# Optimization experiments

Measured on AMD Instinct MI355X. Metric: run time of the kernel, lower is better.

Reference implementation:

```python
import jax, jax.numpy as jnp
import numpy as np

N_EMBD = 2048
N_HEAD = 16
N_KV_HEAD = 4
HEAD_DIM = N_EMBD // N_HEAD  # 128
N_REP = N_HEAD // N_KV_HEAD  # 4
ROPE_BASE = 1000000.0
B, T = 2, 2048


def _rotate_half(x):
    x1, x2 = jnp.split(x, 2, axis=-1)
    return jnp.concatenate([-x2, x1], axis=-1)


def _rope(q, k, t):
    # q: [b,t,h,d], k: [b,t,kvh,d]; full rotary (partial_rotary_factor=1.0)
    pos = jnp.arange(t, dtype=jnp.float32)
    inv_freq = 1.0 / (ROPE_BASE ** (jnp.arange(0, HEAD_DIM, 2, dtype=jnp.float32) / HEAD_DIM))
    ang = pos[:, None] * inv_freq[None, :]                      # [t, d/2]
    cos = jnp.concatenate([jnp.cos(ang), jnp.cos(ang)], -1)     # [t, d]
    sin = jnp.concatenate([jnp.sin(ang), jnp.sin(ang)], -1)
    cos = cos[None, :, None, :]
    sin = sin[None, :, None, :]
    q = q * cos + _rotate_half(q) * sin
    k = k * cos + _rotate_half(k) * sin
    return q, k


def setup_inputs() -> dict:
    key = jax.random.key(0)
    ks = jax.random.split(key, 9)
    std = 0.02
    proj_std = 0.02 / np.sqrt(2 * 24)
    return {
        "x": jax.random.normal(ks[0], (B, T, N_EMBD), dtype=jnp.float32),
        "Wq": jax.random.normal(ks[1], (N_EMBD, N_HEAD * HEAD_DIM), dtype=jnp.float32) * std,
        "bq": jnp.zeros((N_HEAD * HEAD_DIM,), dtype=jnp.float32),
        "Wk": jax.random.normal(ks[2], (N_EMBD, N_KV_HEAD * HEAD_DIM), dtype=jnp.float32) * std,
        "bk": jnp.zeros((N_KV_HEAD * HEAD_DIM,), dtype=jnp.float32),
        "Wv": jax.random.normal(ks[3], (N_EMBD, N_KV_HEAD * HEAD_DIM), dtype=jnp.float32) * std,
        "bv": jnp.zeros((N_KV_HEAD * HEAD_DIM,), dtype=jnp.float32),
        "Wo": jax.random.normal(ks[4], (N_EMBD, N_EMBD), dtype=jnp.float32) * proj_std,
        "bo": jnp.zeros((N_EMBD,), dtype=jnp.float32),
    }


def reference(x, Wq, bq, Wk, bk, Wv, bv, Wo, bo):
    b, t, _ = x.shape
    q = (x @ Wq + bq).reshape(b, t, N_HEAD, HEAD_DIM)
    k = (x @ Wk + bk).reshape(b, t, N_KV_HEAD, HEAD_DIM)
    v = (x @ Wv + bv).reshape(b, t, N_KV_HEAD, HEAD_DIM)
    q, k = _rope(q, k, t)
    # repeat_kv: expand kv heads by n_rep
    k = jnp.broadcast_to(k[:, :, :, None, :], (b, t, N_KV_HEAD, N_REP, HEAD_DIM)).reshape(b, t, N_HEAD, HEAD_DIM)
    v = jnp.broadcast_to(v[:, :, :, None, :], (b, t, N_KV_HEAD, N_REP, HEAD_DIM)).reshape(b, t, N_HEAD, HEAD_DIM)
    qh = q.transpose(0, 2, 1, 3)  # [b,h,t,d]
    kh = k.transpose(0, 2, 1, 3)
    vh = v.transpose(0, 2, 1, 3)
    causal = jnp.tril(jnp.ones((t, t), dtype=bool))[None, None]  # [1,1,t,t]
    bias = jnp.where(causal, 0.0, -1e9).astype(jnp.float32)
    scores = jnp.einsum('bhtd,bhTd->bhtT', qh, kh) / jnp.sqrt(jnp.float32(HEAD_DIM))
    attn_w = jax.nn.softmax(scores + bias, axis=-1)
    attn_out = jnp.einsum('bhtT,bhTd->bhtd', attn_w, vh)
    attn = attn_out.transpose(0, 2, 1, 3).reshape(b, t, N_EMBD)
    return attn @ Wo + bo
```

## Files before the change

kernel.cpp:

```cpp
#include <hip/hip_runtime.h>

typedef _Float16 f16x8 __attribute__((ext_vector_type(8)));
typedef _Float16 f16x4 __attribute__((ext_vector_type(4)));
typedef float    f32x4 __attribute__((ext_vector_type(4)));

__device__ __forceinline__ void gload16(const void* g, void* l) {
  __builtin_amdgcn_global_load_lds((const __attribute__((address_space(1))) void*)g,
                                   (__attribute__((address_space(3))) void*)l, 16, 0, 0);
}

__global__ __launch_bounds__(256) void cast_f32_f16(const float* __restrict__ src,
                                                    _Float16* __restrict__ dst, int n4) {
  int i = blockIdx.x * 256 + threadIdx.x;
  if (i < n4) {
    f32x4 v = *(const f32x4*)(src + (size_t)i * 4);
    f16x4 o;
    o[0] = (_Float16)v[0]; o[1] = (_Float16)v[1];
    o[2] = (_Float16)v[2]; o[3] = (_Float16)v[3];
    *(f16x4*)(dst + (size_t)i * 4) = o;
  }
}

__global__ __launch_bounds__(256) void wqkvtrans_kernel(const float* __restrict__ Wq,
                                                        const float* __restrict__ Wk,
                                                        const float* __restrict__ Wv,
                                                        _Float16* __restrict__ dst) {
  const int n0 = blockIdx.x * 64, k0 = blockIdx.y * 64;
  const float* src; int N, nb;
  if (n0 < 2048)      { src = Wq; N = 2048; nb = n0; }
  else if (n0 < 2560) { src = Wk; N = 512;  nb = n0 - 2048; }
  else                { src = Wv; N = 512;  nb = n0 - 2560; }
  __shared__ float tile[64][65];
#pragma unroll
  for (int i = 0; i < 16; ++i) {
    int id = i * 256 + threadIdx.x;
    int kk = id >> 6, nn = id & 63;
    tile[kk][nn] = src[(size_t)(k0 + kk) * N + nb + nn];
  }
  __syncthreads();
#pragma unroll
  for (int i = 0; i < 16; ++i) {
    int id = i * 256 + threadIdx.x;
    int nn = id >> 6, kk = id & 63;
    dst[(size_t)(n0 + nn) * 2048 + k0 + kk] = (_Float16)tile[kk][nn];
  }
}

__global__ __launch_bounds__(256) void wtrans_kernel(const float* __restrict__ src,
                                                     _Float16* __restrict__ dst,
                                                     int N, int K, int rowOff, int ldDst) {
  const int n0 = blockIdx.x * 64, k0 = blockIdx.y * 64;
  __shared__ float tile[64][65];
#pragma unroll
  for (int i = 0; i < 16; ++i) {
    int id = i * 256 + threadIdx.x;
    int kk = id >> 6, nn = id & 63;
    tile[kk][nn] = src[(size_t)(k0 + kk) * N + n0 + nn];
  }
  __syncthreads();
#pragma unroll
  for (int i = 0; i < 16; ++i) {
    int id = i * 256 + threadIdx.x;
    int nn = id >> 6, kk = id & 63;
    dst[(size_t)(rowOff + n0 + nn) * ldDst + k0 + kk] = (_Float16)tile[kk][nn];
  }
}

__global__ __launch_bounds__(256) void biaspack_kernel(const float* __restrict__ bq,
                                                       const float* __restrict__ bk,
                                                       const float* __restrict__ bv,
                                                       float* __restrict__ out) {
  int i = blockIdx.x * 256 + threadIdx.x;
  if (i < 3072) out[i] = (i < 2048) ? bq[i] : (i < 2560 ? bk[i - 2048] : bv[i - 2560]);
}

template <bool F16OUT>
__global__ __launch_bounds__(256) void gemm_nt(const _Float16* __restrict__ A,
                                               const _Float16* __restrict__ B,
                                               const float* __restrict__ bias,
                                               void* __restrict__ Cv,
                                               int M, int N, int K) {
  __shared__ __align__(16) _Float16 As[128][64];
  __shared__ __align__(16) _Float16 Bs[128][64];
  const int tid = threadIdx.x;
  const int lane = tid & 63, wave = tid >> 6;
  const int wr = wave >> 1, wc = wave & 1;
  const int r = lane & 15, g = lane >> 4;
  const int rb = blockIdx.y * 128, cb = blockIdx.x * 128;

  const int swz = ((tid & 7) ^ ((tid >> 3) & 7)) * 8;
  const _Float16* aSrc = A + (size_t)(rb + (tid >> 3)) * K + swz;
  const _Float16* bSrc = B + (size_t)(cb + (tid >> 3)) * K + swz;

  f32x4 acc[4][4] = {};

  for (int kt = 0; kt < K; kt += 64) {
    __syncthreads();
#pragma unroll
    for (int p = 0; p < 4; ++p) {
      gload16(aSrc + (size_t)(p * 32) * K + kt, (_Float16*)As + (p * 256 + wave * 64) * 8);
      gload16(bSrc + (size_t)(p * 32) * K + kt, (_Float16*)Bs + (p * 256 + wave * 64) * 8);
    }
    __syncthreads();
#pragma unroll
    for (int kk = 0; kk < 2; ++kk) {
      f16x8 af[4], bf[4];
#pragma unroll
      for (int m = 0; m < 4; ++m) {
        int row = wr * 64 + m * 16 + r;
        af[m] = *(const f16x8*)(&As[row][((kk * 4 + g) ^ (row & 7)) * 8]);
      }
#pragma unroll
      for (int n = 0; n < 4; ++n) {
        int row = wc * 64 + n * 16 + r;
        bf[n] = *(const f16x8*)(&Bs[row][((kk * 4 + g) ^ (row & 7)) * 8]);
      }
#pragma unroll
      for (int m = 0; m < 4; ++m)
#pragma unroll
        for (int n = 0; n < 4; ++n)
          acc[m][n] = __builtin_amdgcn_mfma_f32_16x16x32_f16(af[m], bf[n], acc[m][n], 0, 0, 0);
    }
  }

  float bvals[4];
#pragma unroll
  for (int n = 0; n < 4; ++n) bvals[n] = bias[cb + wc * 64 + n * 16 + r];
#pragma unroll
  for (int m = 0; m < 4; ++m) {
#pragma unroll
    for (int n = 0; n < 4; ++n) {
#pragma unroll
      for (int j = 0; j < 4; ++j) {
        int row = rb + wr * 64 + m * 16 + g * 4 + j;
        int col = cb + wc * 64 + n * 16 + r;
        float v = acc[m][n][j] + bvals[n];
        if (F16OUT)
          ((_Float16*)Cv)[(size_t)row * N + col] = (_Float16)v;
        else
          ((float*)Cv)[(size_t)row * N + col] = v;
      }
    }
  }
}

__global__ __launch_bounds__(256) void rope_kernel(_Float16* __restrict__ QKV) {
  const int tok = blockIdx.x;
  const int t = tok & 2047;
  __shared__ float cs[64], sn[64];
  if (threadIdx.x < 64) {
    int j = threadIdx.x;
    float freq = exp2f((float)(-2 * j) * (19.931568569324174f / 128.0f));
    float ang = (float)t * freq;
    cs[j] = cosf(ang);
    sn[j] = sinf(ang);
  }
  __syncthreads();
  _Float16* base = QKV + (size_t)tok * 3072;
  int idx = threadIdx.x;
  if (idx < 160) {
    int head = idx >> 3, j0 = (idx & 7) * 8;
    int cb = (head < 16) ? head * 128 : 2048 + (head - 16) * 128;
    _Float16* p = base + cb;
    f16x8 a = *(const f16x8*)(p + j0);
    f16x8 b2 = *(const f16x8*)(p + 64 + j0);
    f16x8 oa, ob;
#pragma unroll
    for (int e = 0; e < 8; ++e) {
      float c = cs[j0 + e], s = sn[j0 + e];
      float x1 = (float)a[e], x2 = (float)b2[e];
      oa[e] = (_Float16)(x1 * c - x2 * s);
      ob[e] = (_Float16)(x2 * c + x1 * s);
    }
    *(f16x8*)(p + j0) = oa;
    *(f16x8*)(p + 64 + j0) = ob;
  }
}

__global__ __launch_bounds__(256) void vtrans_kernel(const _Float16* __restrict__ QKV,
                                                     _Float16* __restrict__ Vt) {
  const int bk = blockIdx.z;
  const int t0 = blockIdx.x * 64, d0 = blockIdx.y * 64;
  const int b = bk >> 2, kvh = bk & 3;
  __shared__ _Float16 tile[64][65];
  const _Float16* src = QKV + (size_t)b * 2048 * 3072 + 2560 + kvh * 128;
#pragma unroll
  for (int i = 0; i < 16; ++i) {
    int id = i * 256 + threadIdx.x;
    int tt = id >> 6, dd = id & 63;
    tile[tt][dd] = src[(size_t)(t0 + tt) * 3072 + d0 + dd];
  }
  __syncthreads();
  _Float16* dst = Vt + (size_t)bk * 128 * 2048;
#pragma unroll
  for (int i = 0; i < 16; ++i) {
    int id = i * 256 + threadIdx.x;
    int dd = id >> 6, tt = id & 63;
    dst[(size_t)(d0 + dd) * 2048 + t0 + tt] = tile[tt][dd];
  }
}

__global__ __launch_bounds__(512) void attn_kernel(const _Float16* __restrict__ QKV,
                                                   const _Float16* __restrict__ Vt,
                                                   _Float16* __restrict__ O) {
  const int bid = blockIdx.x;
  const int b = bid >> 8;
  const int ii = bid & 255;
  const int h = ii >> 4;
  const int qtr = ii & 15;
  const int qt = b ? 15 - qtr : qtr;
  const int tid = threadIdx.x;
  const int wave = tid >> 6, lane = tid & 63;
  const int r = lane & 15, g = lane >> 4;
  const int q0 = qt * 128 + wave * 16;
  const int kvh = h >> 2;
  const _Float16* Qb  = QKV + (size_t)b * 2048 * 3072 + h * 128;
  const _Float16* Kb  = QKV + (size_t)b * 2048 * 3072 + 2048 + kvh * 128;
  const _Float16* Vtg = Vt + (size_t)(b * 4 + kvh) * 128 * 2048;

  __shared__ __align__(16) _Float16 Klds[2][64][128];
  __shared__ __align__(16) _Float16 Vlds[2][128][64];
  __shared__ __align__(16) _Float16 Plds[8][16][64];

  const _Float16* kSrc = Kb  + (size_t)(tid >> 4) * 3072 + (((tid & 15) ^ ((tid >> 4) & 7)) * 8);
  const _Float16* vSrc = Vtg + (size_t)(tid >> 3) * 2048 + (((tid & 7) ^ ((tid >> 3) & 7)) * 8);

  f16x8 qf[4];
  {
    const float qsc = 0.08838834764831845f * 1.4426950408889634f;
    const _Float16* qrow = Qb + (size_t)(q0 + r) * 3072 + g * 8;
#pragma unroll
    for (int c = 0; c < 4; ++c) {
      f16x8 v = *(const f16x8*)(qrow + c * 32);
#pragma unroll
      for (int i = 0; i < 8; ++i) v[i] = (_Float16)((float)v[i] * qsc);
      qf[c] = v;
    }
  }
  asm volatile("s_waitcnt vmcnt(0)" ::: "memory");

  f32x4 oacc[8] = {};
  float mrun = -1e30f, lrun = 0.f;
  const int kend = qt * 128 + 128;
  const int qlim = q0 + 16;

  {
    gload16(kSrc,                          &Klds[0][0][0] + (wave * 64) * 8);
    gload16(kSrc + (size_t)32 * 3072,      &Klds[0][0][0] + (512 + wave * 64) * 8);
    gload16(vSrc,                          &Vlds[0][0][0] + (wave * 64) * 8);
    gload16(vSrc + (size_t)64 * 2048,      &Vlds[0][0][0] + (512 + wave * 64) * 8);
  }

  int cur = 0;
  for (int kb = 0; kb < kend; kb += 64) {
    if (kb + 64 < kend) {
      int nb = kb + 64, nxt = cur ^ 1;
      gload16(kSrc + (size_t)nb * 3072,        &Klds[nxt][0][0] + (wave * 64) * 8);
      gload16(kSrc + (size_t)(nb + 32) * 3072, &Klds[nxt][0][0] + (512 + wave * 64) * 8);
      gload16(vSrc + nb,                       &Vlds[nxt][0][0] + (wave * 64) * 8);
      gload16(vSrc + (size_t)64 * 2048 + nb,   &Vlds[nxt][0][0] + (512 + wave * 64) * 8);
      asm volatile("s_waitcnt vmcnt(4)" ::: "memory");
    } else {
      asm volatile("s_waitcnt vmcnt(0)" ::: "memory");
    }
    __builtin_amdgcn_s_barrier();
    __builtin_amdgcn_sched_barrier(0);
    if (kb < qlim) {
      f32x4 sT[4] = {};
      __builtin_amdgcn_s_setprio(1);
#pragma unroll
      for (int c = 0; c < 4; ++c) {
#pragma unroll
        for (int n = 0; n < 4; ++n) {
          f16x8 kf = *(const f16x8*)(&Klds[cur][n * 16 + r][(((c * 4 + g) ^ (r & 7)) * 8)]);
          sT[n] = __builtin_amdgcn_mfma_f32_16x16x32_f16(kf, qf[c], sT[n], 0, 0, 0);
        }
      }
      __builtin_amdgcn_s_setprio(0);
      if (kb + 63 > q0) {
#pragma unroll
        for (int n = 0; n < 4; ++n)
#pragma unroll
          for (int j = 0; j < 4; ++j) {
            int kg = kb + n * 16 + g * 4 + j;
            if (kg > q0 + r) sT[n][j] = -1e30f;
          }
      }
      float mt = -1e30f;
#pragma unroll
      for (int n = 0; n < 4; ++n)
#pragma unroll
        for (int j = 0; j < 4; ++j) mt = fmaxf(mt, sT[n][j]);
      mt = fmaxf(mt, __shfl_xor(mt, 16));
      mt = fmaxf(mt, __shfl_xor(mt, 32));
      if (__any(mt > mrun)) {
        float mnew = fmaxf(mrun, mt);
        float alpha = exp2f(mrun - mnew);
        lrun *= alpha;
        float al[4];
#pragma unroll
        for (int jj = 0; jj < 4; ++jj) al[jj] = __shfl(alpha, g * 4 + jj);
#pragma unroll
        for (int dt = 0; dt < 8; ++dt)
#pragma unroll
          for (int jj = 0; jj < 4; ++jj) oacc[dt][jj] *= al[jj];
        mrun = mnew;
      }
      float p[4][4];
      float rs = 0.f;
#pragma unroll
      for (int n = 0; n < 4; ++n)
#pragma unroll
        for (int j = 0; j < 4; ++j) {
          p[n][j] = exp2f(sT[n][j] - mrun);
          rs += p[n][j];
        }
      rs += __shfl_xor(rs, 16);
      rs += __shfl_xor(rs, 32);
      lrun += rs;
      asm volatile("" ::: "memory");
#pragma unroll
      for (int n = 0; n < 4; ++n) {
        f16x4 p4;
#pragma unroll
        for (int j = 0; j < 4; ++j) p4[j] = (_Float16)p[n][j];
        int c16s = (2 * n + (g >> 1)) ^ (r & 7);
        *(f16x4*)(&Plds[wave][r][c16s * 8 + (g & 1) * 4]) = p4;
      }
      asm volatile("s_waitcnt lgkmcnt(0)" ::: "memory");
      __builtin_amdgcn_sched_barrier(0);
      f16x8 pa0 = *(const f16x8*)(&Plds[wave][r][((g) ^ (r & 7)) * 8]);
      f16x8 pa1 = *(const f16x8*)(&Plds[wave][r][((4 + g) ^ (r & 7)) * 8]);
      __builtin_amdgcn_s_setprio(1);
#pragma unroll
      for (int dt = 0; dt < 8; ++dt) {
        f16x8 vf0 = *(const f16x8*)(&Vlds[cur][dt * 16 + r][((g) ^ (r & 7)) * 8]);
        oacc[dt] = __builtin_amdgcn_mfma_f32_16x16x32_f16(pa0, vf0, oacc[dt], 0, 0, 0);
        f16x8 vf1 = *(const f16x8*)(&Vlds[cur][dt * 16 + r][((4 + g) ^ (r & 7)) * 8]);
        oacc[dt] = __builtin_amdgcn_mfma_f32_16x16x32_f16(pa1, vf1, oacc[dt], 0, 0, 0);
      }
      __builtin_amdgcn_s_setprio(0);
    }
    __builtin_amdgcn_sched_barrier(0);
    __builtin_amdgcn_s_barrier();
    __builtin_amdgcn_sched_barrier(0);
    cur ^= 1;
  }

  float linv = 1.0f / lrun;
  float li[4];
#pragma unroll
  for (int jj = 0; jj < 4; ++jj) li[jj] = __shfl(linv, g * 4 + jj);
#pragma unroll
  for (int dt = 0; dt < 8; ++dt)
#pragma unroll
    for (int jj = 0; jj < 4; ++jj)
      O[(size_t)(b * 2048 + q0 + g * 4 + jj) * 2048 + h * 128 + dt * 16 + r] =
          (_Float16)(oacc[dt][jj] * li[jj]);
}

extern "C" void kernel_launch(void* const* d_in, const int* in_sizes, int n_in,
                              void* d_out, int out_size, void* d_ws, size_t ws_size,
                              hipStream_t stream) {
  const float* x  = (const float*)d_in[0];
  const float* Wq = (const float*)d_in[1];
  const float* bq = (const float*)d_in[2];
  const float* Wk = (const float*)d_in[3];
  const float* bk = (const float*)d_in[4];
  const float* Wv = (const float*)d_in[5];
  const float* bv = (const float*)d_in[6];
  const float* Wo = (const float*)d_in[7];
  const float* bo = (const float*)d_in[8];
  float* out = (float*)d_out;

  char* ws = (char*)d_ws;
  constexpr size_t QKV_OFF  = 0;
  constexpr size_t VT_OFF   = 25165824;
  constexpr size_t ATTN_OFF = VT_OFF + 4194304;
  constexpr size_t WT_OFF   = ATTN_OFF + 16777216;
  constexpr size_t BIAS_OFF = WT_OFF + 12582912;
  _Float16* QKV  = (_Float16*)(ws + QKV_OFF);
  _Float16* Vt   = (_Float16*)(ws + VT_OFF);
  _Float16* attn = (_Float16*)(ws + ATTN_OFF);
  _Float16* WT   = (_Float16*)(ws + WT_OFF);
  float*    bqkv = (float*)(ws + BIAS_OFF);
  _Float16* xb = (_Float16*)d_out;

  cast_f32_f16<<<8192, 256, 0, stream>>>(x, xb, (2 * 2048 * 2048) / 4);
  wqkvtrans_kernel<<<dim3(48, 32), 256, 0, stream>>>(Wq, Wk, Wv, WT);
  biaspack_kernel<<<12, 256, 0, stream>>>(bq, bk, bv, bqkv);
  gemm_nt<true><<<dim3(3072 / 128, 4096 / 128), 256, 0, stream>>>(xb, WT, bqkv, QKV, 4096, 3072, 2048);
  wtrans_kernel<<<dim3(32, 32), 256, 0, stream>>>(Wo, WT, 2048, 2048, 0, 2048);
  rope_kernel<<<4096, 256, 0, stream>>>(QKV);
  vtrans_kernel<<<dim3(32, 2, 8), 256, 0, stream>>>(QKV, Vt);
  attn_kernel<<<512, 512, 0, stream>>>(QKV, Vt, attn);
  gemm_nt<false><<<dim3(2048 / 128, 4096 / 128), 256, 0, stream>>>(attn, WT, bo, out, 4096, 2048, 2048);
}
```

Before: 216.6 us.

## Switch attention to 32x32x16 MFMA with 4 waves of 32 query rows

```diff
diff --git a/kernel.cpp b/kernel.cpp
--- a/kernel.cpp
+++ b/kernel.cpp
@@ -3,6 +3,7 @@
 typedef _Float16 f16x8 __attribute__((ext_vector_type(8)));
 typedef _Float16 f16x4 __attribute__((ext_vector_type(4)));
 typedef float    f32x4 __attribute__((ext_vector_type(4)));
+typedef float    f32x16 __attribute__((ext_vector_type(16)));
 
 __device__ __forceinline__ void gload16(const void* g, void* l) {
   __builtin_amdgcn_global_load_lds((const __attribute__((address_space(1))) void*)g,
@@ -200,7 +201,7 @@
   }
 }
 
-__global__ __launch_bounds__(512) void attn_kernel(const _Float16* __restrict__ QKV,
+__global__ __launch_bounds__(256) void attn_kernel(const _Float16* __restrict__ QKV,
                                                    const _Float16* __restrict__ Vt,
                                                    _Float16* __restrict__ O) {
   const int bid = blockIdx.x;
@@ -211,152 +212,133 @@
   const int qt = b ? 15 - qtr : qtr;
   const int tid = threadIdx.x;
   const int wave = tid >> 6, lane = tid & 63;
-  const int r = lane & 15, g = lane >> 4;
-  const int q0 = qt * 128 + wave * 16;
+  const int l31 = lane & 31, hi = lane >> 5;
+  const int q0w = qt * 128 + wave * 32;
   const int kvh = h >> 2;
   const _Float16* Qb  = QKV + (size_t)b * 2048 * 3072 + h * 128;
   const _Float16* Kb  = QKV + (size_t)b * 2048 * 3072 + 2048 + kvh * 128;
   const _Float16* Vtg = Vt + (size_t)(b * 4 + kvh) * 128 * 2048;
 
-  __shared__ __align__(16) _Float16 Klds[2][64][128];
-  __shared__ __align__(16) _Float16 Vlds[2][128][64];
-  __shared__ __align__(16) _Float16 Plds[8][16][64];
+  __shared__ __align__(16) _Float16 Klds[64][128];
+  __shared__ __align__(16) _Float16 Vlds[128][64];
+  __shared__ __align__(16) _Float16 Plds[4][32][64];
 
   const _Float16* kSrc = Kb  + (size_t)(tid >> 4) * 3072 + (((tid & 15) ^ ((tid >> 4) & 7)) * 8);
   const _Float16* vSrc = Vtg + (size_t)(tid >> 3) * 2048 + (((tid & 7) ^ ((tid >> 3) & 7)) * 8);
 
-  f16x8 qf[4];
+  f16x8 qf[8];
   {
     const float qsc = 0.08838834764831845f * 1.4426950408889634f;
-    const _Float16* qrow = Qb + (size_t)(q0 + r) * 3072 + g * 8;
-#pragma unroll
-    for (int c = 0; c < 4; ++c) {
-      f16x8 v = *(const f16x8*)(qrow + c * 32);
-#pragma unroll
-      for (int i = 0; i < 8; ++i) v[i] = (_Float16)((float)v[i] * qsc);
-      qf[c] = v;
-    }
-  }
-  asm volatile("s_waitcnt vmcnt(0)" ::: "memory");
-
-  f32x4 oacc[8] = {};
+    const _Float16* qrow = Qb + (size_t)(q0w + l31) * 3072 + hi * 8;
+#pragma unroll
+    for (int ds = 0; ds < 8; ++ds) {
+      f16x8 v = *(const f16x8*)(qrow + ds * 16);
+#pragma unroll
+      for (int e = 0; e < 8; ++e) v[e] = (_Float16)((float)v[e] * qsc);
+      qf[ds] = v;
+    }
+  }
+
+  f32x16 oacc[4] = {};
   float mrun = -1e30f, lrun = 0.f;
   const int kend = qt * 128 + 128;
-  const int qlim = q0 + 16;
-
-  {
-    gload16(kSrc,                          &Klds[0][0][0] + (wave * 64) * 8);
-    gload16(kSrc + (size_t)32 * 3072,      &Klds[0][0][0] + (512 + wave * 64) * 8);
-    gload16(vSrc,                          &Vlds[0][0][0] + (wave * 64) * 8);
-    gload16(vSrc + (size_t)64 * 2048,      &Vlds[0][0][0] + (512 + wave * 64) * 8);
-  }
-
-  int cur = 0;
+  const int qlim = q0w + 32;
+
   for (int kb = 0; kb < kend; kb += 64) {
-    if (kb + 64 < kend) {
-      int nb = kb + 64, nxt = cur ^ 1;
-      gload16(kSrc + (size_t)nb * 3072,        &Klds[nxt][0][0] + (wave * 64) * 8);
-      gload16(kSrc + (size_t)(nb + 32) * 3072, &Klds[nxt][0][0] + (512 + wave * 64) * 8);
-      gload16(vSrc + nb,                       &Vlds[nxt][0][0] + (wave * 64) * 8);
-      gload16(vSrc + (size_t)64 * 2048 + nb,   &Vlds[nxt][0][0] + (512 + wave * 64) * 8);
-      asm volatile("s_waitcnt vmcnt(4)" ::: "memory");
-    } else {
-      asm volatile("s_waitcnt vmcnt(0)" ::: "memory");
-    }
-    __builtin_amdgcn_s_barrier();
-    __builtin_amdgcn_sched_barrier(0);
+#pragma unroll
+    for (int p = 0; p < 4; ++p) {
+      gload16(kSrc + (size_t)(kb + p * 16) * 3072, (_Float16*)Klds + (p * 256 + tid) * 8);
+      gload16(vSrc + (size_t)(p * 32) * 2048 + kb, (_Float16*)Vlds + (p * 256 + tid) * 8);
+    }
+    __syncthreads();
     if (kb < qlim) {
-      f32x4 sT[4] = {};
+      f32x16 sT[2] = {};
       __builtin_amdgcn_s_setprio(1);
 #pragma unroll
-      for (int c = 0; c < 4; ++c) {
-#pragma unroll
-        for (int n = 0; n < 4; ++n) {
-          f16x8 kf = *(const f16x8*)(&Klds[cur][n * 16 + r][(((c * 4 + g) ^ (r & 7)) * 8)]);
-          sT[n] = __builtin_amdgcn_mfma_f32_16x16x32_f16(kf, qf[c], sT[n], 0, 0, 0);
+      for (int ds = 0; ds < 8; ++ds) {
+#pragma unroll
+        for (int ks = 0; ks < 2; ++ks) {
+          f16x8 kf = *(const f16x8*)(&Klds[ks * 32 + l31][(((ds * 2 + hi) ^ (l31 & 7)) * 8)]);
+          sT[ks] = __builtin_amdgcn_mfma_f32_32x32x16_f16(kf, qf[ds], sT[ks], 0, 0, 0);
         }
       }
       __builtin_amdgcn_s_setprio(0);
-      if (kb + 63 > q0) {
-#pragma unroll
-        for (int n = 0; n < 4; ++n)
-#pragma unroll
-          for (int j = 0; j < 4; ++j) {
-            int kg = kb + n * 16 + g * 4 + j;
-            if (kg > q0 + r) sT[n][j] = -1e30f;
+      if (kb + 63 > q0w) {
+#pragma unroll
+        for (int ks = 0; ks < 2; ++ks)
+#pragma unroll
+          for (int r = 0; r < 16; ++r) {
+            int kg = kb + ks * 32 + (r & 3) + 8 * (r >> 2) + 4 * hi;
+            if (kg > q0w + l31) sT[ks][r] = -1e30f;
           }
       }
       float mt = -1e30f;
 #pragma unroll
-      for (int n = 0; n < 4; ++n)
-#pragma unroll
-        for (int j = 0; j < 4; ++j) mt = fmaxf(mt, sT[n][j]);
-      mt = fmaxf(mt, __shfl_xor(mt, 16));
+      for (int ks = 0; ks < 2; ++ks)
+#pragma unroll
+        for (int r = 0; r < 16; ++r) mt = fmaxf(mt, sT[ks][r]);
       mt = fmaxf(mt, __shfl_xor(mt, 32));
       if (__any(mt > mrun)) {
         float mnew = fmaxf(mrun, mt);
         float alpha = exp2f(mrun - mnew);
         lrun *= alpha;
-        float al[4];
-#pragma unroll
-        for (int jj = 0; jj < 4; ++jj) al[jj] = __shfl(alpha, g * 4 + jj);
-#pragma unroll
-        for (int dt = 0; dt < 8; ++dt)
-#pragma unroll
-          for (int jj = 0; jj < 4; ++jj) oacc[dt][jj] *= al[jj];
+#pragma unroll
+        for (int r = 0; r < 16; ++r) {
+          float al = __shfl(alpha, (r & 3) + 8 * (r >> 2) + 4 * hi);
+#pragma unroll
+          for (int dsub = 0; dsub < 4; ++dsub) oacc[dsub][r] *= al;
+        }
         mrun = mnew;
       }
-      float p[4][4];
+      float pv[2][16];
       float rs = 0.f;
 #pragma unroll
-      for (int n = 0; n < 4; ++n)
-#pragma unroll
-        for (int j = 0; j < 4; ++j) {
-          p[n][j] = exp2f(sT[n][j] - mrun);
-          rs += p[n][j];
-        }
-      rs += __shfl_xor(rs, 16);
+      for (int ks = 0; ks < 2; ++ks)
+#pragma unroll
+        for (int r = 0; r < 16; ++r) {
+          pv[ks][r] = exp2f(sT[ks][r] - mrun);
+          rs += pv[ks][r];
+        }
       rs += __shfl_xor(rs, 32);
       lrun += rs;
       asm volatile("" ::: "memory");
 #pragma unroll
-      for (int n = 0; n < 4; ++n) {
-        f16x4 p4;
-#pragma unroll
-        for (int j = 0; j < 4; ++j) p4[j] = (_Float16)p[n][j];
-        int c16s = (2 * n + (g >> 1)) ^ (r & 7);
-        *(f16x4*)(&Plds[wave][r][c16s * 8 + (g & 1) * 4]) = p4;
-      }
+      for (int ks = 0; ks < 2; ++ks)
+#pragma unroll
+        for (int m = 0; m < 4; ++m) {
+          f16x4 w;
+#pragma unroll
+          for (int j = 0; j < 4; ++j) w[j] = (_Float16)pv[ks][m * 4 + j];
+          int c = (ks * 4 + m) ^ (l31 & 7);
+          *(f16x4*)(&Plds[wave][l31][c * 8 + hi * 4]) = w;
+        }
       asm volatile("s_waitcnt lgkmcnt(0)" ::: "memory");
       __builtin_amdgcn_sched_barrier(0);
-      f16x8 pa0 = *(const f16x8*)(&Plds[wave][r][((g) ^ (r & 7)) * 8]);
-      f16x8 pa1 = *(const f16x8*)(&Plds[wave][r][((4 + g) ^ (r & 7)) * 8]);
       __builtin_amdgcn_s_setprio(1);
 #pragma unroll
-      for (int dt = 0; dt < 8; ++dt) {
-        f16x8 vf0 = *(const f16x8*)(&Vlds[cur][dt * 16 + r][((g) ^ (r & 7)) * 8]);
-        oacc[dt] = __builtin_amdgcn_mfma_f32_16x16x32_f16(pa0, vf0, oacc[dt], 0, 0, 0);
-        f16x8 vf1 = *(const f16x8*)(&Vlds[cur][dt * 16 + r][((4 + g) ^ (r & 7)) * 8]);
-        oacc[dt] = __builtin_amdgcn_mfma_f32_16x16x32_f16(pa1, vf1, oacc[dt], 0, 0, 0);
+      for (int s = 0; s < 4; ++s) {
+        f16x8 pa = *(const f16x8*)(&Plds[wave][l31][(((s * 2 + hi) ^ (l31 & 7)) * 8)]);
+#pragma unroll
+        for (int dsub = 0; dsub < 4; ++dsub) {
+          f16x8 vf = *(const f16x8*)(&Vlds[dsub * 32 + l31][(((s * 2 + hi) ^ (l31 & 7)) * 8)]);
+          oacc[dsub] = __builtin_amdgcn_mfma_f32_32x32x16_f16(pa, vf, oacc[dsub], 0, 0, 0);
+        }
       }
       __builtin_amdgcn_s_setprio(0);
     }
-    __builtin_amdgcn_sched_barrier(0);
-    __builtin_amdgcn_s_barrier();
-    __builtin_amdgcn_sched_barrier(0);
-    cur ^= 1;
+    __syncthreads();
   }
 
   float linv = 1.0f / lrun;
-  float li[4];
-#pragma unroll
-  for (int jj = 0; jj < 4; ++jj) li[jj] = __shfl(linv, g * 4 + jj);
-#pragma unroll
-  for (int dt = 0; dt < 8; ++dt)
-#pragma unroll
-    for (int jj = 0; jj < 4; ++jj)
-      O[(size_t)(b * 2048 + q0 + g * 4 + jj) * 2048 + h * 128 + dt * 16 + r] =
-          (_Float16)(oacc[dt][jj] * li[jj]);
+#pragma unroll
+  for (int r = 0; r < 16; ++r) {
+    int qrow = (r & 3) + 8 * (r >> 2) + 4 * hi;
+    float li = __shfl(linv, qrow);
+    _Float16* orow = O + (size_t)(b * 2048 + q0w + qrow) * 2048 + h * 128 + l31;
+#pragma unroll
+    for (int dsub = 0; dsub < 4; ++dsub)
+      orow[dsub * 32] = (_Float16)(oacc[dsub][r] * li);
+  }
 }
 
 extern "C" void kernel_launch(void* const* d_in, const int* in_sizes, int n_in,
@@ -393,6 +375,6 @@
   wtrans_kernel<<<dim3(32, 32), 256, 0, stream>>>(Wo, WT, 2048, 2048, 0, 2048);
   rope_kernel<<<4096, 256, 0, stream>>>(QKV);
   vtrans_kernel<<<dim3(32, 2, 8), 256, 0, stream>>>(QKV, Vt);
-  attn_kernel<<<512, 512, 0, stream>>>(QKV, Vt, attn);
+  attn_kernel<<<512, 256, 0, stream>>>(QKV, Vt, attn);
   gemm_nt<false><<<dim3(2048 / 128, 4096 / 128), 256, 0, stream>>>(attn, WT, bo, out, 4096, 2048, 2048);
 }
```

After: 277.0 us. 27.9% more time.

## Use persistent atomic work queue with smaller 64-row query tiles in attention

Applied to the files above, without the earlier changes.

```diff
diff --git a/kernel.cpp b/kernel.cpp
--- a/kernel.cpp
+++ b/kernel.cpp
@@ -73,6 +73,8 @@
   int i = blockIdx.x * 256 + threadIdx.x;
   if (i < 3072) out[i] = (i < 2048) ? bq[i] : (i < 2560 ? bk[i - 2048] : bv[i - 2560]);
 }
+
+__global__ void zeroctr_kernel(int* c) { *c = 0; }
 
 template <bool F16OUT>
 __global__ __launch_bounds__(256) void gemm_nt(const _Float16* __restrict__ A,
@@ -200,163 +202,154 @@
   }
 }
 
-__global__ __launch_bounds__(512) void attn_kernel(const _Float16* __restrict__ QKV,
+__global__ __launch_bounds__(256) void attn_kernel(const _Float16* __restrict__ QKV,
                                                    const _Float16* __restrict__ Vt,
-                                                   _Float16* __restrict__ O) {
-  const int bid = blockIdx.x;
-  const int b = bid >> 8;
-  const int ii = bid & 255;
-  const int h = ii >> 4;
-  const int qtr = ii & 15;
-  const int qt = b ? 15 - qtr : qtr;
+                                                   _Float16* __restrict__ O,
+                                                   int* __restrict__ ctr) {
   const int tid = threadIdx.x;
   const int wave = tid >> 6, lane = tid & 63;
   const int r = lane & 15, g = lane >> 4;
-  const int q0 = qt * 128 + wave * 16;
-  const int kvh = h >> 2;
-  const _Float16* Qb  = QKV + (size_t)b * 2048 * 3072 + h * 128;
-  const _Float16* Kb  = QKV + (size_t)b * 2048 * 3072 + 2048 + kvh * 128;
-  const _Float16* Vtg = Vt + (size_t)(b * 4 + kvh) * 128 * 2048;
-
-  __shared__ __align__(16) _Float16 Klds[2][64][128];
-  __shared__ __align__(16) _Float16 Vlds[2][128][64];
-  __shared__ __align__(16) _Float16 Plds[8][16][64];
-
-  const _Float16* kSrc = Kb  + (size_t)(tid >> 4) * 3072 + (((tid & 15) ^ ((tid >> 4) & 7)) * 8);
-  const _Float16* vSrc = Vtg + (size_t)(tid >> 3) * 2048 + (((tid & 7) ^ ((tid >> 3) & 7)) * 8);
-
-  f16x8 qf[4];
-  {
-    const float qsc = 0.08838834764831845f * 1.4426950408889634f;
-    const _Float16* qrow = Qb + (size_t)(q0 + r) * 3072 + g * 8;
-#pragma unroll
-    for (int c = 0; c < 4; ++c) {
-      f16x8 v = *(const f16x8*)(qrow + c * 32);
-#pragma unroll
-      for (int i = 0; i < 8; ++i) v[i] = (_Float16)((float)v[i] * qsc);
-      qf[c] = v;
-    }
-  }
-  asm volatile("s_waitcnt vmcnt(0)" ::: "memory");
-
-  f32x4 oacc[8] = {};
-  float mrun = -1e30f, lrun = 0.f;
-  const int kend = qt * 128 + 128;
-  const int qlim = q0 + 16;
-
-  {
-    gload16(kSrc,                          &Klds[0][0][0] + (wave * 64) * 8);
-    gload16(kSrc + (size_t)32 * 3072,      &Klds[0][0][0] + (512 + wave * 64) * 8);
-    gload16(vSrc,                          &Vlds[0][0][0] + (wave * 64) * 8);
-    gload16(vSrc + (size_t)64 * 2048,      &Vlds[0][0][0] + (512 + wave * 64) * 8);
-  }
-
-  int cur = 0;
-  for (int kb = 0; kb < kend; kb += 64) {
-    if (kb + 64 < kend) {
-      int nb = kb + 64, nxt = cur ^ 1;
-      gload16(kSrc + (size_t)nb * 3072,        &Klds[nxt][0][0] + (wave * 64) * 8);
-      gload16(kSrc + (size_t)(nb + 32) * 3072, &Klds[nxt][0][0] + (512 + wave * 64) * 8);
-      gload16(vSrc + nb,                       &Vlds[nxt][0][0] + (wave * 64) * 8);
-      gload16(vSrc + (size_t)64 * 2048 + nb,   &Vlds[nxt][0][0] + (512 + wave * 64) * 8);
-      asm volatile("s_waitcnt vmcnt(4)" ::: "memory");
-    } else {
-      asm volatile("s_waitcnt vmcnt(0)" ::: "memory");
-    }
-    __builtin_amdgcn_s_barrier();
-    __builtin_amdgcn_sched_barrier(0);
-    if (kb < qlim) {
-      f32x4 sT[4] = {};
-      __builtin_amdgcn_s_setprio(1);
+
+  __shared__ __align__(16) _Float16 Klds[64][128];
+  __shared__ __align__(16) _Float16 Vlds[128][64];
+  __shared__ __align__(16) _Float16 Plds[4][16][64];
+  __shared__ int wslot;
+
+  const int kRowOff = tid >> 4, kChunk = ((tid & 15) ^ ((tid >> 4) & 7)) * 8;
+  const int vRowOff = tid >> 3, vChunk = ((tid & 7) ^ ((tid >> 3) & 7)) * 8;
+
+  for (;;) {
+    __syncthreads();
+    if (tid == 0) wslot = atomicAdd(ctr, 1);
+    __syncthreads();
+    const int w = wslot;
+    if (w >= 1024) break;
+    const int qt = 31 - (w >> 5);
+    const int rem = w & 31;
+    const int b = rem >> 4, h = rem & 15;
+    const int kvh = h >> 2;
+    const int q0 = qt * 64 + wave * 16;
+    const _Float16* Qb  = QKV + (size_t)b * 2048 * 3072 + h * 128;
+    const _Float16* Kb  = QKV + (size_t)b * 2048 * 3072 + 2048 + kvh * 128;
+    const _Float16* Vtg = Vt + (size_t)(b * 4 + kvh) * 128 * 2048;
+    const _Float16* kSrc = Kb  + (size_t)kRowOff * 3072 + kChunk;
+    const _Float16* vSrc = Vtg + (size_t)vRowOff * 2048 + vChunk;
+
+    f16x8 qf[4];
+    {
+      const float qsc = 0.08838834764831845f * 1.4426950408889634f;
+      const _Float16* qrow = Qb + (size_t)(q0 + r) * 3072 + g * 8;
 #pragma unroll
       for (int c = 0; c < 4; ++c) {
+        f16x8 v = *(const f16x8*)(qrow + c * 32);
+#pragma unroll
+        for (int i = 0; i < 8; ++i) v[i] = (_Float16)((float)v[i] * qsc);
+        qf[c] = v;
+      }
+    }
+
+    f32x4 oacc[8] = {};
+    float mrun = -1e30f, lrun = 0.f;
+    const int kend = qt * 64 + 64;
+    const int qlim = q0 + 16;
+
+    for (int kb = 0; kb < kend; kb += 64) {
+#pragma unroll
+      for (int p = 0; p < 4; ++p) {
+        gload16(kSrc + (size_t)(kb + p * 16) * 3072, (_Float16*)Klds + (p * 256 + wave * 64) * 8);
+        gload16(vSrc + (size_t)(p * 32) * 2048 + kb, (_Float16*)Vlds + (p * 256 + wave * 64) * 8);
+      }
+      __syncthreads();
+      if (kb < qlim) {
+        f32x4 sT[4] = {};
+        __builtin_amdgcn_s_setprio(1);
+#pragma unroll
+        for (int c = 0; c < 4; ++c) {
+#pragma unroll
+          for (int n = 0; n < 4; ++n) {
+            f16x8 kf = *(const f16x8*)(&Klds[n * 16 + r][(((c * 4 + g) ^ (r & 7)) * 8)]);
+            sT[n] = __builtin_amdgcn_mfma_f32_16x16x32_f16(kf, qf[c], sT[n], 0, 0, 0);
+          }
+        }
+        __builtin_amdgcn_s_setprio(0);
+        if (kb + 63 > q0) {
+#pragma unroll
+          for (int n = 0; n < 4; ++n)
+#pragma unroll
+            for (int j = 0; j < 4; ++j) {
+              int kg = kb + n * 16 + g * 4 + j;
+              if (kg > q0 + r) sT[n][j] = -1e30f;
+            }
+        }
+        float mt = -1e30f;
+#pragma unroll
+        for (int n = 0; n < 4; ++n)
+#pragma unroll
+          for (int j = 0; j < 4; ++j) mt = fmaxf(mt, sT[n][j]);
+        mt = fmaxf(mt, __shfl_xor(mt, 16));
+        mt = fmaxf(mt, __shfl_xor(mt, 32));
+        if (__any(mt > mrun)) {
+          float mnew = fmaxf(mrun, mt);
+          float alpha = exp2f(mrun - mnew);
+          lrun *= alpha;
+          float al[4];
+#pragma unroll
+          for (int jj = 0; jj < 4; ++jj) al[jj] = __shfl(alpha, g * 4 + jj);
+#pragma unroll
+          for (int dt = 0; dt < 8; ++dt)
+#pragma unroll
+            for (int jj = 0; jj < 4; ++jj) oacc[dt][jj] *= al[jj];
+          mrun = mnew;
+        }
+        float p[4][4];
+        float rs = 0.f;
+#pragma unroll
+        for (int n = 0; n < 4; ++n)
+#pragma unroll
+          for (int j = 0; j < 4; ++j) {
+            p[n][j] = exp2f(sT[n][j] - mrun);
+            rs += p[n][j];
+          }
+        rs += __shfl_xor(rs, 16);
+        rs += __shfl_xor(rs, 32);
+        lrun += rs;
+        asm volatile("" ::: "memory");
 #pragma unroll
         for (int n = 0; n < 4; ++n) {
-          f16x8 kf = *(const f16x8*)(&Klds[cur][n * 16 + r][(((c * 4 + g) ^ (r & 7)) * 8)]);
-          sT[n] = __builtin_amdgcn_mfma_f32_16x16x32_f16(kf, qf[c], sT[n], 0, 0, 0);
-        }
-      }
-      __builtin_amdgcn_s_setprio(0);
-      if (kb + 63 > q0) {
-#pragma unroll
-        for (int n = 0; n < 4; ++n)
-#pragma unroll
-          for (int j = 0; j < 4; ++j) {
-            int kg = kb + n * 16 + g * 4 + j;
-            if (kg > q0 + r) sT[n][j] = -1e30f;
-          }
-      }
-      float mt = -1e30f;
-#pragma unroll
-      for (int n = 0; n < 4; ++n)
-#pragma unroll
-        for (int j = 0; j < 4; ++j) mt = fmaxf(mt, sT[n][j]);
-      mt = fmaxf(mt, __shfl_xor(mt, 16));
-      mt = fmaxf(mt, __shfl_xor(mt, 32));
-      if (__any(mt > mrun)) {
-        float mnew = fmaxf(mrun, mt);
-        float alpha = exp2f(mrun - mnew);
-        lrun *= alpha;
-        float al[4];
-#pragma unroll
-        for (int jj = 0; jj < 4; ++jj) al[jj] = __shfl(alpha, g * 4 + jj);
-#pragma unroll
-        for (int dt = 0; dt < 8; ++dt)
-#pragma unroll
-          for (int jj = 0; jj < 4; ++jj) oacc[dt][jj] *= al[jj];
-        mrun = mnew;
-      }
-      float p[4][4];
-      float rs = 0.f;
-#pragma unroll
-      for (int n = 0; n < 4; ++n)
-#pragma unroll
-        for (int j = 0; j < 4; ++j) {
-          p[n][j] = exp2f(sT[n][j] - mrun);
-          rs += p[n][j];
-        }
-      rs += __shfl_xor(rs, 16);
-      rs += __shfl_xor(rs, 32);
-      lrun += rs;
-      asm volatile("" ::: "memory");
-#pragma unroll
-      for (int n = 0; n < 4; ++n) {
-        f16x4 p4;
-#pragma unroll
-        for (int j = 0; j < 4; ++j) p4[j] = (_Float16)p[n][j];
-        int c16s = (2 * n + (g >> 1)) ^ (r & 7);
-        *(f16x4*)(&Plds[wave][r][c16s * 8 + (g & 1) * 4]) = p4;
-      }
-      asm volatile("s_waitcnt lgkmcnt(0)" ::: "memory");
-      __builtin_amdgcn_sched_barrier(0);
-      f16x8 pa0 = *(const f16x8*)(&Plds[wave][r][((g) ^ (r & 7)) * 8]);
-      f16x8 pa1 = *(const f16x8*)(&Plds[wave][r][((4 + g) ^ (r & 7)) * 8]);
-      __builtin_amdgcn_s_setprio(1);
-#pragma unroll
-      for (int dt = 0; dt < 8; ++dt) {
-        f16x8 vf0 = *(const f16x8*)(&Vlds[cur][dt * 16 + r][((g) ^ (r & 7)) * 8]);
-        oacc[dt] = __builtin_amdgcn_mfma_f32_16x16x32_f16(pa0, vf0, oacc[dt], 0, 0, 0);
-        f16x8 vf1 = *(const f16x8*)(&Vlds[cur][dt * 16 + r][((4 + g) ^ (r & 7)) * 8]);
-        oacc[dt] = __builtin_amdgcn_mfma_f32_16x16x32_f16(pa1, vf1, oacc[dt], 0, 0, 0);
-      }
-      __builtin_amdgcn_s_setprio(0);
-    }
-    __builtin_amdgcn_sched_barrier(0);
-    __builtin_amdgcn_s_barrier();
-    __builtin_amdgcn_sched_barrier(0);
-    cur ^= 1;
-  }
-
-  float linv = 1.0f / lrun;
-  float li[4];
-#pragma unroll
-  for (int jj = 0; jj < 4; ++jj) li[jj] = __shfl(linv, g * 4 + jj);
-#pragma unroll
-  for (int dt = 0; dt < 8; ++dt)
-#pragma unroll
-    for (int jj = 0; jj < 4; ++jj)
-      O[(size_t)(b * 2048 + q0 + g * 4 + jj) * 2048 + h * 128 + dt * 16 + r] =
-          (_Float16)(oacc[dt][jj] * li[jj]);
+          f16x4 p4;
+#pragma unroll
+          for (int j = 0; j < 4; ++j) p4[j] = (_Float16)p[n][j];
+          int c16s = (2 * n + (g >> 1)) ^ (r & 7);
+          *(f16x4*)(&Plds[wave][r][c16s * 8 + (g & 1) * 4]) = p4;
+        }
+        asm volatile("s_waitcnt lgkmcnt(0)" ::: "memory");
+        __builtin_amdgcn_sched_barrier(0);
+        f16x8 pa0 = *(const f16x8*)(&Plds[wave][r][((g) ^ (r & 7)) * 8]);
+        f16x8 pa1 = *(const f16x8*)(&Plds[wave][r][((4 + g) ^ (r & 7)) * 8]);
+        __builtin_amdgcn_s_setprio(1);
+#pragma unroll
+        for (int dt = 0; dt < 8; ++dt) {
+          f16x8 vf0 = *(const f16x8*)(&Vlds[dt * 16 + r][((g) ^ (r & 7)) * 8]);
+          oacc[dt] = __builtin_amdgcn_mfma_f32_16x16x32_f16(pa0, vf0, oacc[dt], 0, 0, 0);
+          f16x8 vf1 = *(const f16x8*)(&Vlds[dt * 16 + r][((4 + g) ^ (r & 7)) * 8]);
+          oacc[dt] = __builtin_amdgcn_mfma_f32_16x16x32_f16(pa1, vf1, oacc[dt], 0, 0, 0);
+        }
+        __builtin_amdgcn_s_setprio(0);
+      }
+      __syncthreads();
+    }
+
+    float linv = 1.0f / lrun;
+    float li[4];
+#pragma unroll
+    for (int jj = 0; jj < 4; ++jj) li[jj] = __shfl(linv, g * 4 + jj);
+#pragma unroll
+    for (int dt = 0; dt < 8; ++dt)
+#pragma unroll
+      for (int jj = 0; jj < 4; ++jj)
+        O[(size_t)(b * 2048 + q0 + g * 4 + jj) * 2048 + h * 128 + dt * 16 + r] =
+            (_Float16)(oacc[dt][jj] * li[jj]);
+  }
 }
 
 extern "C" void kernel_launch(void* const* d_in, const int* in_sizes, int n_in,
@@ -379,20 +372,23 @@
   constexpr size_t ATTN_OFF = VT_OFF + 4194304;
   constexpr size_t WT_OFF   = ATTN_OFF + 16777216;
   constexpr size_t BIAS_OFF = WT_OFF + 12582912;
+  constexpr size_t CTR_OFF  = BIAS_OFF + 12288;
   _Float16* QKV  = (_Float16*)(ws + QKV_OFF);
   _Float16* Vt   = (_Float16*)(ws + VT_OFF);
   _Float16* attn = (_Float16*)(ws + ATTN_OFF);
   _Float16* WT   = (_Float16*)(ws + WT_OFF);
   float*    bqkv = (float*)(ws + BIAS_OFF);
+  int*      ctr  = (int*)(ws + CTR_OFF);
   _Float16* xb = (_Float16*)d_out;
 
   cast_f32_f16<<<8192, 256, 0, stream>>>(x, xb, (2 * 2048 * 2048) / 4);
   wqkvtrans_kernel<<<dim3(48, 32), 256, 0, stream>>>(Wq, Wk, Wv, WT);
   biaspack_kernel<<<12, 256, 0, stream>>>(bq, bk, bv, bqkv);
+  zeroctr_kernel<<<1, 1, 0, stream>>>(ctr);
   gemm_nt<true><<<dim3(3072 / 128, 4096 / 128), 256, 0, stream>>>(xb, WT, bqkv, QKV, 4096, 3072, 2048);
   wtrans_kernel<<<dim3(32, 32), 256, 0, stream>>>(Wo, WT, 2048, 2048, 0, 2048);
   rope_kernel<<<4096, 256, 0, stream>>>(QKV);
   vtrans_kernel<<<dim3(32, 2, 8), 256, 0, stream>>>(QKV, Vt);
-  attn_kernel<<<512, 512, 0, stream>>>(QKV, Vt, attn);
+  attn_kernel<<<1024, 256, 0, stream>>>(QKV, Vt, attn, ctr);
   gemm_nt<false><<<dim3(2048 / 128, 4096 / 128), 256, 0, stream>>>(attn, WT, bo, out, 4096, 2048, 2048);
 }
```

Result: slower. 226.4 us (+4.5%).

## Replace double-buffered 64-key attention tiles with single-buffered 128-key tiles

Applied to the files above, without the earlier changes.

```diff
diff --git a/kernel.cpp b/kernel.cpp
--- a/kernel.cpp
+++ b/kernel.cpp
@@ -218,12 +218,14 @@
   const _Float16* Kb  = QKV + (size_t)b * 2048 * 3072 + 2048 + kvh * 128;
   const _Float16* Vtg = Vt + (size_t)(b * 4 + kvh) * 128 * 2048;
 
-  __shared__ __align__(16) _Float16 Klds[2][64][128];
-  __shared__ __align__(16) _Float16 Vlds[2][128][64];
+  __shared__ __align__(16) _Float16 Klds[128][128];
+  __shared__ __align__(16) _Float16 Vlds[128][128];
   __shared__ __align__(16) _Float16 Plds[8][16][64];
 
-  const _Float16* kSrc = Kb  + (size_t)(tid >> 4) * 3072 + (((tid & 15) ^ ((tid >> 4) & 7)) * 8);
-  const _Float16* vSrc = Vtg + (size_t)(tid >> 3) * 2048 + (((tid & 7) ^ ((tid >> 3) & 7)) * 8);
+  const int sRow = tid >> 4;
+  const int sChunk = ((tid & 15) ^ ((tid >> 4) & 7)) * 8;
+  const _Float16* kSrc = Kb  + (size_t)sRow * 3072 + sChunk;
+  const _Float16* vSrc = Vtg + (size_t)sRow * 2048 + sChunk;
 
   f16x8 qf[4];
   {
@@ -237,52 +239,40 @@
       qf[c] = v;
     }
   }
-  asm volatile("s_waitcnt vmcnt(0)" ::: "memory");
 
   f32x4 oacc[8] = {};
   float mrun = -1e30f, lrun = 0.f;
   const int kend = qt * 128 + 128;
   const int qlim = q0 + 16;
 
-  {
-    gload16(kSrc,                          &Klds[0][0][0] + (wave * 64) * 8);
-    gload16(kSrc + (size_t)32 * 3072,      &Klds[0][0][0] + (512 + wave * 64) * 8);
-    gload16(vSrc,                          &Vlds[0][0][0] + (wave * 64) * 8);
-    gload16(vSrc + (size_t)64 * 2048,      &Vlds[0][0][0] + (512 + wave * 64) * 8);
-  }
-
-  int cur = 0;
-  for (int kb = 0; kb < kend; kb += 64) {
-    if (kb + 64 < kend) {
-      int nb = kb + 64, nxt = cur ^ 1;
-      gload16(kSrc + (size_t)nb * 3072,        &Klds[nxt][0][0] + (wave * 64) * 8);
-      gload16(kSrc + (size_t)(nb + 32) * 3072, &Klds[nxt][0][0] + (512 + wave * 64) * 8);
-      gload16(vSrc + nb,                       &Vlds[nxt][0][0] + (wave * 64) * 8);
-      gload16(vSrc + (size_t)64 * 2048 + nb,   &Vlds[nxt][0][0] + (512 + wave * 64) * 8);
-      asm volatile("s_waitcnt vmcnt(4)" ::: "memory");
-    } else {
-      asm volatile("s_waitcnt vmcnt(0)" ::: "memory");
-    }
-    __builtin_amdgcn_s_barrier();
-    __builtin_amdgcn_sched_barrier(0);
-    if (kb < qlim) {
+  for (int kb = 0; kb < kend; kb += 128) {
+#pragma unroll
+    for (int p = 0; p < 4; ++p) {
+      gload16(kSrc + (size_t)(kb + p * 32) * 3072, (_Float16*)Klds + (p * 512 + tid) * 8);
+      gload16(vSrc + (size_t)(p * 32) * 2048 + kb, (_Float16*)Vlds + (p * 512 + tid) * 8);
+    }
+    __syncthreads();
+#pragma unroll
+    for (int kk2 = 0; kk2 < 128; kk2 += 64) {
+      const int kbb = kb + kk2;
+      if (kbb >= qlim) break;
       f32x4 sT[4] = {};
       __builtin_amdgcn_s_setprio(1);
 #pragma unroll
       for (int c = 0; c < 4; ++c) {
 #pragma unroll
         for (int n = 0; n < 4; ++n) {
-          f16x8 kf = *(const f16x8*)(&Klds[cur][n * 16 + r][(((c * 4 + g) ^ (r & 7)) * 8)]);
+          f16x8 kf = *(const f16x8*)(&Klds[kk2 + n * 16 + r][(((c * 4 + g) ^ (r & 7)) * 8)]);
           sT[n] = __builtin_amdgcn_mfma_f32_16x16x32_f16(kf, qf[c], sT[n], 0, 0, 0);
         }
       }
       __builtin_amdgcn_s_setprio(0);
-      if (kb + 63 > q0) {
+      if (kbb + 63 > q0) {
 #pragma unroll
         for (int n = 0; n < 4; ++n)
 #pragma unroll
           for (int j = 0; j < 4; ++j) {
-            int kg = kb + n * 16 + g * 4 + j;
+            int kg = kbb + n * 16 + g * 4 + j;
             if (kg > q0 + r) sT[n][j] = -1e30f;
           }
       }
@@ -334,17 +324,14 @@
       __builtin_amdgcn_s_setprio(1);
 #pragma unroll
       for (int dt = 0; dt < 8; ++dt) {
-        f16x8 vf0 = *(const f16x8*)(&Vlds[cur][dt * 16 + r][((g) ^ (r & 7)) * 8]);
+        f16x8 vf0 = *(const f16x8*)(&Vlds[dt * 16 + r][((((kk2 >> 3) + g) ^ (r & 7)) * 8)]);
         oacc[dt] = __builtin_amdgcn_mfma_f32_16x16x32_f16(pa0, vf0, oacc[dt], 0, 0, 0);
-        f16x8 vf1 = *(const f16x8*)(&Vlds[cur][dt * 16 + r][((4 + g) ^ (r & 7)) * 8]);
+        f16x8 vf1 = *(const f16x8*)(&Vlds[dt * 16 + r][((((kk2 >> 3) + 4 + g) ^ (r & 7)) * 8)]);
         oacc[dt] = __builtin_amdgcn_mfma_f32_16x16x32_f16(pa1, vf1, oacc[dt], 0, 0, 0);
       }
       __builtin_amdgcn_s_setprio(0);
     }
-    __builtin_amdgcn_sched_barrier(0);
-    __builtin_amdgcn_s_barrier();
-    __builtin_amdgcn_sched_barrier(0);
-    cur ^= 1;
+    __syncthreads();
   }
 
   float linv = 1.0f / lrun;
```

After: 214.8 us. Within noise of the previous version (-0.9%).
